# Optimization experiments

Hardware: AMD Instinct MI355X
Metric: run time of the kernel (lower is better)

Reference implementation:

```python
import jax, jax.numpy as jnp
import numpy as np

BM = 192  # query block size (kernel hard-coded to BM=192)


def setup_inputs() -> dict:
    key = jax.random.key(0)
    k1, k2, k3 = jax.random.split(key, 3)
    B, H, S, D = 1, 12, 3840, 128
    q = jax.random.normal(k1, (B, H, S, D), dtype=jnp.float32)
    k = jax.random.normal(k2, (B, H, S, D), dtype=jnp.float32)
    v = jax.random.normal(k3, (B, H, S, D), dtype=jnp.float32)
    topk = 1024
    return {"q": q, "k": k, "v": v, "topk": topk}


def reference(q, k, v, topk):
    # Chipmunk SparseDiffAttn core pipeline:
    # 1) dense_colsum_attn: dense attention whose probs are column-summed per
    #    192-query block to produce block scores bs [B,H,QG,S]
    # 2) topk index selection per query group (mask -> indices)
    # 3) csp_attn: block-sparse attention where each 192-query group attends
    #    only to its selected top-k keys
    B, H, S, D = q.shape
    QG = S // BM
    scale = 1.0 / np.sqrt(D)

    # --- dense colsum attention (scoring pass) ---
    scores = jnp.einsum('bhqd,bhkd->bhqk', q, k) * scale      # [B,H,S,S]
    probs = jax.nn.softmax(scores, axis=-1)                   # [B,H,S,S]
    # column-sum of attention probs within each 192-query block
    bs = probs.reshape(B, H, QG, BM, S).sum(axis=-2)          # [B,H,QG,S]

    # --- topk mask -> per-group key indices ---
    _, inds = jax.lax.top_k(bs, topk)                         # [B,H,QG,TK] int32

    # --- block-sparse gather attention (csp_attn) ---
    # gather selected keys/values per query group
    gather = jax.vmap(jax.vmap(lambda kv, idx: kv[idx]))      # over B, H
    kg = gather(k, inds)                                      # [B,H,QG,TK,D]
    vg = gather(v, inds)                                      # [B,H,QG,TK,D]
    qg = q.reshape(B, H, QG, BM, D)                           # [B,H,QG,BM,D]

    s2 = jnp.einsum('bhgqd,bhgkd->bhgqk', qg, kg) * scale     # [B,H,QG,BM,TK]
    p2 = jax.nn.softmax(s2, axis=-1)
    o = jnp.einsum('bhgqk,bhgkd->bhgqd', p2, vg)              # [B,H,QG,BM,D]
    return o.reshape(B, H, S, D)
```

## Files before the change

kernel.cpp:

```cpp
#include <hip/hip_runtime.h>
#include <math.h>


#define HH 12
#define SS 3840
#define DD 128
#define QGn 20
#define TKn 1024
#define NROWS (HH * QGn)
#define HS (HH * SS)
#define NT 60
#define TCH 3072
#define SCALE_D 0.08838834764831845
#define SCALE_F 0.08838834764831845f

typedef short short8 __attribute__((ext_vector_type(8)));
typedef float f32x4 __attribute__((ext_vector_type(4)));

#define MFMA(a, b, c) __builtin_amdgcn_mfma_f32_16x16x32_bf16(a, b, c, 0, 0, 0)
#define MFMA_B16(c, a, b) \
  c = __builtin_amdgcn_mfma_f32_16x16x32_bf16(a, b, c, 0, 0, 0)

typedef __attribute__((address_space(3))) unsigned int lds_u32;
typedef const __attribute__((address_space(1))) unsigned int glb_u32;

__device__ __forceinline__ unsigned short bf_rne(float x) {
  unsigned u = __float_as_uint(x);
  u = (u + 0x7fffu + ((u >> 16) & 1u)) >> 16;
  return (unsigned short)u;
}
__device__ __forceinline__ float bf_f(unsigned short b) {
  return __uint_as_float(((unsigned)b) << 16);
}
__device__ __forceinline__ void split3(float f, unsigned short& a,
                                       unsigned short& b, unsigned short& c) {
  a = bf_rne(f);
  float r = f - bf_f(a);
  b = bf_rne(r);
  r = r - bf_f(b);
  c = bf_rne(r);
}
__device__ __forceinline__ void split2(float f, unsigned short& a,
                                       unsigned short& b) {
  a = bf_rne(f);
  float r = f - bf_f(a);
  b = bf_rne(r);
}
__device__ __forceinline__ short8 ldfrag(const unsigned short* base, int chunk) {
  return *(const short8*)&base[(size_t)chunk * 8];
}

__global__ __launch_bounds__(1024) void presplit_kernel(
    const float* __restrict__ q, const float* __restrict__ k,
    unsigned short* __restrict__ qsplit, unsigned short* __restrict__ ksplit) {
  const int t = threadIdx.x;
  const int lane = t & 63;
  const int u = t >> 6;
  const int kc = u & 3, kt = u >> 2;
  const int ln = lane & 15, quad = lane >> 4;
  const int c = blockIdx.x;
  const int h = blockIdx.y;
  const float* src = blockIdx.z ? k : q;
  unsigned short* dst = blockIdx.z ? ksplit : qsplit;

  const float* p =
      &src[(size_t)(h * SS + c * 64 + kt * 16 + ln) * DD + kc * 32 + quad * 8];
  float b8[8];
  *(float4*)&b8[0] = *(const float4*)&p[0];
  *(float4*)&b8[4] = *(const float4*)&p[4];
  unsigned short f0[8], f1[8], f2[8];
#pragma unroll
  for (int e = 0; e < 8; ++e) split3(b8[e], f0[e], f1[e], f2[e]);
  size_t base =
      ((size_t)(h * NT + c) * TCH + ((kt * 4 + kc) * 3) * 64 + lane) * 8;
  *(ushort4*)&dst[base + 0] = *(ushort4*)&f0[0];
  *(ushort4*)&dst[base + 4] = *(ushort4*)&f0[4];
  *(ushort4*)&dst[base + 512] = *(ushort4*)&f1[0];
  *(ushort4*)&dst[base + 516] = *(ushort4*)&f1[4];
  *(ushort4*)&dst[base + 1024] = *(ushort4*)&f2[0];
  *(ushort4*)&dst[base + 1028] = *(ushort4*)&f2[4];
}

__global__ __launch_bounds__(256) void stats_mfma(
    const unsigned short* __restrict__ qsplit,
    const unsigned short* __restrict__ ksplit,
    double* __restrict__ lpart) {
  __shared__ __align__(16) unsigned short Bs[3][6144];
  const int t = threadIdx.x;
  const int w = t >> 6;
  const int lane = t & 63;
  const int ln = lane & 15;
  const int quad = lane >> 4;
  const int h = blockIdx.y;
  const int nq = blockIdx.z;
  const int q0 = blockIdx.x * 128 + w * 32;
  const int tq = blockIdx.x * 2 + (w >> 1);
  const int ktA = (w & 1) * 2;

  short8 A[2][4][3];
  {
    const unsigned short* qb = &qsplit[(size_t)(h * NT + tq) * TCH * 8];
#pragma unroll
    for (int s = 0; s < 2; ++s)
#pragma unroll
      for (int kc = 0; kc < 4; ++kc)
#pragma unroll
        for (int cm = 0; cm < 3; ++cm)
          A[s][kc][cm] =
              ldfrag(qb, (((ktA + s) * 4 + kc) * 3 + cm) * 64 + lane);
  }

  double racc[2][4];
#pragma unroll
  for (int s = 0; s < 2; ++s)
#pragma unroll
    for (int r = 0; r < 4; ++r) racc[s][r] = 0.0;

  const unsigned short* kq = &ksplit[(size_t)(h * NT + nq * 15) * TCH * 8];

#define STG_S(slot, j)                                                     \
  do {                                                                     \
    const unsigned short* src_ = kq + (size_t)(j) * 6144 + t * 8;          \
    __builtin_amdgcn_global_load_lds((glb_u32*)(src_),                     \
        (lds_u32*)&Bs[slot][w * 512], 16, 0, 0);                           \
    __builtin_amdgcn_global_load_lds((glb_u32*)(src_ + 2048),              \
        (lds_u32*)&Bs[slot][2048 + w * 512], 16, 0, 0);                    \
    __builtin_amdgcn_global_load_lds((glb_u32*)(src_ + 4096),              \
        (lds_u32*)&Bs[slot][4096 + w * 512], 16, 0, 0);                    \
  } while (0)

  const f32x4 z = {0.f, 0.f, 0.f, 0.f};
  f32x4 C[2][3];

  STG_S(0, 0);

  int cur = 0;
#pragma unroll 1
  for (int j = 0; j < 60; ++j) {
    __builtin_amdgcn_sched_barrier(0);
    if (j < 59) {
      const int nxt = (cur == 2) ? 0 : cur + 1;
      STG_S(nxt, j + 1);
      asm volatile("s_waitcnt vmcnt(3)" ::: "memory");
    } else {
      asm volatile("s_waitcnt vmcnt(0)" ::: "memory");
    }
    __builtin_amdgcn_s_barrier();
    __builtin_amdgcn_sched_barrier(0);
    __builtin_amdgcn_s_setprio(1);
    if (j > 0) {
#pragma unroll
      for (int s = 0; s < 2; ++s)
#pragma unroll
        for (int r = 0; r < 4; ++r) {
          float sv = (C[s][0][r] + C[s][1][r]) + C[s][2][r];
          racc[s][r] += (double)__expf(sv * SCALE_F);
        }
    }
    const unsigned short* Bp = &Bs[cur][0];
#pragma unroll
    for (int kc = 0; kc < 4; ++kc) {
      short8 B0 = *(const short8*)&Bp[(kc * 3 + 0) * 512 + lane * 8];
      short8 B1 = *(const short8*)&Bp[(kc * 3 + 1) * 512 + lane * 8];
      short8 B2 = *(const short8*)&Bp[(kc * 3 + 2) * 512 + lane * 8];
#pragma unroll
      for (int s = 0; s < 2; ++s) {
        if (kc == 0) {
          C[s][0] = MFMA(A[s][0][0], B0, z);
          C[s][1] = MFMA(A[s][0][0], B1, z);
          C[s][1] = MFMA(A[s][0][1], B0, C[s][1]);
          C[s][0] = MFMA(A[s][0][1], B1, C[s][0]);
          C[s][2] = MFMA(A[s][0][2], B0, z);
          C[s][2] = MFMA(A[s][0][0], B2, C[s][2]);
        } else {
          MFMA_B16(C[s][0], A[s][kc][0], B0);
          MFMA_B16(C[s][1], A[s][kc][0], B1);
          MFMA_B16(C[s][1], A[s][kc][1], B0);
          MFMA_B16(C[s][0], A[s][kc][1], B1);
          MFMA_B16(C[s][2], A[s][kc][2], B0);
          MFMA_B16(C[s][2], A[s][kc][0], B2);
        }
      }
    }
    __builtin_amdgcn_s_setprio(0);
    cur = (cur == 2) ? 0 : cur + 1;
  }
#undef STG_S

#pragma unroll
  for (int s = 0; s < 2; ++s)
#pragma unroll
    for (int r = 0; r < 4; ++r) {
      float sv = (C[s][0][r] + C[s][1][r]) + C[s][2][r];
      racc[s][r] += (double)__expf(sv * SCALE_F);
    }

#pragma unroll
  for (int s = 0; s < 2; ++s)
#pragma unroll
    for (int r = 0; r < 4; ++r) {
      double v = racc[s][r];
      v += __shfl_xor(v, 1);
      v += __shfl_xor(v, 2);
      v += __shfl_xor(v, 4);
      v += __shfl_xor(v, 8);
      if (ln == 0)
        lpart[(size_t)nq * HS + h * SS + q0 + s * 16 + quad * 4 + r] = v;
    }
}

__global__ __launch_bounds__(256) void colsum_mfma(
    const unsigned short* __restrict__ qsplit,
    const unsigned short* __restrict__ ksplit,
    const double* __restrict__ lpart, double* __restrict__ bs) {
  __shared__ double rls[192];
  __shared__ __align__(16) unsigned short As[3][6144];
  const int t = threadIdx.x;
  const int w = t >> 6;
  const int lane = t & 63;
  const int ln = lane & 15;
  const int quad = lane >> 4;
  const int h = blockIdx.z, g = blockIdx.y;
  const int k0 = blockIdx.x * 128 + w * 32;
  const int tk = blockIdx.x * 2 + (w >> 1);
  const int ktB = (w & 1) * 2;

  short8 Bk[2][4][3];
  {
    const unsigned short* kb = &ksplit[(size_t)(h * NT + tk) * TCH * 8];
#pragma unroll
    for (int s = 0; s < 2; ++s)
#pragma unroll
      for (int kc = 0; kc < 4; ++kc)
#pragma unroll
        for (int cm = 0; cm < 3; ++cm)
          Bk[s][kc][cm] =
              ldfrag(kb, (((ktB + s) * 4 + kc) * 3 + cm) * 64 + lane);
  }

  if (t < 192) {
    size_t qi = h * SS + g * 192 + t;
    rls[t] = 1.0 / (lpart[qi] + lpart[HS + qi] + lpart[2 * (size_t)HS + qi] +
                    lpart[3 * (size_t)HS + qi]);
  }
  __syncthreads();

  double cacc[2] = {0.0, 0.0};

  const unsigned short* qg = &qsplit[(size_t)(h * NT + g * 3) * TCH * 8];

#define STG_C(slot, j)                                                     \
  do {                                                                     \
    const unsigned short* src_ = qg + (size_t)(j) * 6144 + t * 8;          \
    __builtin_amdgcn_global_load_lds((glb_u32*)(src_),                     \
        (lds_u32*)&As[slot][w * 512], 16, 0, 0);                           \
    __builtin_amdgcn_global_load_lds((glb_u32*)(src_ + 2048),              \
        (lds_u32*)&As[slot][2048 + w * 512], 16, 0, 0);                    \
    __builtin_amdgcn_global_load_lds((glb_u32*)(src_ + 4096),              \
        (lds_u32*)&As[slot][4096 + w * 512], 16, 0, 0);                    \
  } while (0)

  const f32x4 z = {0.f, 0.f, 0.f, 0.f};
  f32x4 C[2][3];

  STG_C(0, 0);

  int cur = 0;
#pragma unroll 1
  for (int j = 0; j < 12; ++j) {
    __builtin_amdgcn_sched_barrier(0);
    if (j < 11) {
      const int nxt = (cur == 2) ? 0 : cur + 1;
      STG_C(nxt, j + 1);
      asm volatile("s_waitcnt vmcnt(3)" ::: "memory");
    } else {
      asm volatile("s_waitcnt vmcnt(0)" ::: "memory");
    }
    __builtin_amdgcn_s_barrier();
    __builtin_amdgcn_sched_barrier(0);
    __builtin_amdgcn_s_setprio(1);
    if (j > 0) {
      const int qprev = (j - 1) * 16;
#pragma unroll
      for (int s = 0; s < 2; ++s)
#pragma unroll
        for (int r = 0; r < 4; ++r) {
          float p = __expf(((C[s][0][r] + C[s][1][r]) + C[s][2][r]) * SCALE_F);
          cacc[s] += (double)p * rls[qprev + quad * 4 + r];
        }
    }
    const unsigned short* Ap = &As[cur][0];
#pragma unroll
    for (int kc = 0; kc < 4; ++kc) {
      short8 A0 = *(const short8*)&Ap[(kc * 3 + 0) * 512 + lane * 8];
      short8 A1 = *(const short8*)&Ap[(kc * 3 + 1) * 512 + lane * 8];
      short8 A2 = *(const short8*)&Ap[(kc * 3 + 2) * 512 + lane * 8];
#pragma unroll
      for (int s = 0; s < 2; ++s) {
        if (kc == 0) {
          C[s][0] = MFMA(A0, Bk[s][0][0], z);
          C[s][1] = MFMA(A1, Bk[s][0][0], z);
          C[s][1] = MFMA(A0, Bk[s][0][1], C[s][1]);
          C[s][0] = MFMA(A1, Bk[s][0][1], C[s][0]);
          C[s][2] = MFMA(A2, Bk[s][0][0], z);
          C[s][2] = MFMA(A0, Bk[s][0][2], C[s][2]);
        } else {
          MFMA_B16(C[s][0], A0, Bk[s][kc][0]);
          MFMA_B16(C[s][1], A1, Bk[s][kc][0]);
          MFMA_B16(C[s][1], A0, Bk[s][kc][1]);
          MFMA_B16(C[s][0], A1, Bk[s][kc][1]);
          MFMA_B16(C[s][2], A2, Bk[s][kc][0]);
          MFMA_B16(C[s][2], A0, Bk[s][kc][2]);
        }
      }
    }
    __builtin_amdgcn_s_setprio(0);
    cur = (cur == 2) ? 0 : cur + 1;
  }
#undef STG_C

#pragma unroll
  for (int s = 0; s < 2; ++s)
#pragma unroll
    for (int r = 0; r < 4; ++r) {
      float p = __expf(((C[s][0][r] + C[s][1][r]) + C[s][2][r]) * SCALE_F);
      cacc[s] += (double)p * rls[176 + quad * 4 + r];
    }

#pragma unroll
  for (int s = 0; s < 2; ++s) {
    double v = cacc[s];
    v += __shfl_xor(v, 16);
    v += __shfl_xor(v, 32);
    if (quad == 0)
      bs[(size_t)(h * QGn + g) * SS + k0 + s * 16 + ln] = v;
  }
}

__global__ __launch_bounds__(256) void topk3_kernel(
    const double* __restrict__ bs, int* __restrict__ inds,
    double* __restrict__ bnd_val, int* __restrict__ bnd_idx) {
  __shared__ unsigned long long u[SS];
  __shared__ int hist[256];
  __shared__ int sfx[256];
  __shared__ int s_bin, s_r;
  __shared__ int c_gt, c_eq;
  __shared__ unsigned long long rv[256];
  __shared__ int ri[256];
  const int t = threadIdx.x;
  const int row = blockIdx.x;
  const double* vals = bs + (size_t)row * SS;

  for (int i = t; i < SS; i += 256)
    u[i] = (unsigned long long)__double_as_longlong(vals[i]);

  unsigned long long pref = 0ull;
  int r = TKn;
  for (int shift = 56; shift >= 0; shift -= 8) {
    hist[t] = 0;
    __syncthreads();
    unsigned long long himask =
        (shift == 56) ? 0ull : (0xFFFFFFFFFFFFFFFFull << (shift + 8));
    for (int i = t; i < SS; i += 256) {
      unsigned long long uv = u[i];
      if ((uv & himask) == (pref & himask))
        atomicAdd(&hist[(int)((uv >> shift) & 255)], 1);
    }
    __syncthreads();
    sfx[t] = hist[t];
    __syncthreads();
#pragma unroll
    for (int off = 1; off < 256; off <<= 1) {
      int v = (t + off < 256) ? sfx[t + off] : 0;
      __syncthreads();
      sfx[t] += v;
      __syncthreads();
    }
    {
      int St = sfx[t];
      int Sn = (t == 255) ? 0 : sfx[t + 1];
      if (St >= r && Sn < r) {
        s_bin = t;
        s_r = r - Sn;
      }
    }
    if (t == 0) {
      c_gt = 0;
      c_eq = 0;
    }
    __syncthreads();
    pref |= ((unsigned long long)s_bin) << shift;
    r = s_r;
    __syncthreads();
  }
  const int G = TKn - r;
  int* out = inds + (size_t)row * TKn;
  unsigned long long mb = 0ull;
  int mbi = -1;
  for (int i = t; i < SS; i += 256) {
    unsigned long long uv = u[i];
    if (uv > pref) {
      int p = atomicAdd(&c_gt, 1);
      out[p] = i;
    } else if (uv == pref) {
      int e = atomicAdd(&c_eq, 1);
      if (e < r) out[G + e] = i;
      if (e == r - 1) bnd_idx[row * 2 + 0] = i;
    } else if (uv > mb) {
      mb = uv;
      mbi = i;
    }
  }
  rv[t] = mb;
  ri[t] = mbi;
  __syncthreads();
  for (int s2 = 128; s2 > 0; s2 >>= 1) {
    if (t < s2 && rv[t + s2] > rv[t]) {
      rv[t] = rv[t + s2];
      ri[t] = ri[t + s2];
    }
    __syncthreads();
  }
  if (t == 0) {
    bnd_val[row * 2 + 0] = __longlong_as_double((long long)pref);
    bnd_val[row * 2 + 1] = __longlong_as_double((long long)rv[0]);
    bnd_idx[row * 2 + 1] = ri[0];
  }
}

__global__ __launch_bounds__(256) void argmin_kernel(
    const double* __restrict__ bnd_val, const int* __restrict__ bnd_idx,
    int* __restrict__ rsel) {
  __shared__ double gmin[256];
  __shared__ int grow[256];
  const int t = threadIdx.x;
  double g = 1e300;
  int r = -1;
  if (t < NROWS) {
    g = bnd_val[t * 2 + 0] - bnd_val[t * 2 + 1];
    r = t;
  }
  gmin[t] = g;
  grow[t] = r;
  __syncthreads();
  for (int s2 = 128; s2 > 0; s2 >>= 1) {
    if (t < s2 && gmin[t + s2] < gmin[t]) {
      gmin[t] = gmin[t + s2];
      grow[t] = grow[t + s2];
    }
    __syncthreads();
  }
  if (t == 0) {
    int rr = grow[0];
    rsel[0] = rr;
    rsel[1] = bnd_idx[rr * 2 + 0];
    rsel[2] = bnd_idx[rr * 2 + 1];
  }
}

__global__ __launch_bounds__(256) void exact_rl_kernel(
    const float* __restrict__ q, const float* __restrict__ k,
    const int* __restrict__ rsel, double* __restrict__ rl_exact) {
  __shared__ double qd[DD];
  __shared__ double red[256];
  const int t = threadIdx.x;
  const int row = rsel[0];
  const int h = row / QGn, g = row % QGn;
  const float* qp = &q[(size_t)(h * SS + g * 192 + blockIdx.x) * DD];
  if (t < DD) qd[t] = (double)qp[t];
  __syncthreads();
  double l = 0.0;
  for (int kk = t; kk < SS; kk += 256) {
    const float* kp = &k[(size_t)(h * SS + kk) * DD];
    double s = 0.0;
#pragma unroll 4
    for (int d = 0; d < DD; d += 4) {
      float4 kv = *(const float4*)&kp[d];
      s += qd[d] * (double)kv.x + qd[d + 1] * (double)kv.y +
           qd[d + 2] * (double)kv.z + qd[d + 3] * (double)kv.w;
    }
    l += exp(s * SCALE_D);
  }
  red[t] = l;
  __syncthreads();
  for (int s2 = 128; s2 > 0; s2 >>= 1) {
    if (t < s2) red[t] += red[t + s2];
    __syncthreads();
  }
  if (t == 0) rl_exact[blockIdx.x] = 1.0 / red[0];
}

__global__ __launch_bounds__(256) void exact_pair_kernel(
    const float* __restrict__ q, const float* __restrict__ k,
    const int* __restrict__ rsel, const double* __restrict__ rl_exact,
    int* __restrict__ inds) {
  __shared__ double redX[256], redY[256];
  const int t = threadIdx.x;
  const int row = rsel[0], kept = rsel[1], drop = rsel[2];
  const int h = row / QGn, g = row % QGn;
  double px = 0.0, py = 0.0;
  if (t < 192) {
    const float* qp = &q[(size_t)(h * SS + g * 192 + t) * DD];
    const float* kx = &k[(size_t)(h * SS + kept) * DD];
    const float* ky = &k[(size_t)(h * SS + drop) * DD];
    double sx = 0.0, sy = 0.0;
#pragma unroll 4
    for (int d = 0; d < DD; ++d) {
      double qv = (double)qp[d];
      sx += qv * (double)kx[d];
      sy += qv * (double)ky[d];
    }
    double rv = rl_exact[t];
    px = exp(sx * SCALE_D) * rv;
    py = exp(sy * SCALE_D) * rv;
  }
  redX[t] = px;
  redY[t] = py;
  __syncthreads();
  for (int s2 = 128; s2 > 0; s2 >>= 1) {
    if (t < s2) { redX[t] += redX[t + s2]; redY[t] += redY[t + s2]; }
    __syncthreads();
  }
  if (t == 0)
    inds[(size_t)row * TKn + (TKn - 1)] = (redX[0] <= redY[0]) ? kept : drop;
}

__global__ __launch_bounds__(256, 3) void sparse_attn_mfma(
    const float* __restrict__ q, const float* __restrict__ v,
    const int* __restrict__ inds, const unsigned short* __restrict__ ksplit,
    float* __restrict__ out) {
  __shared__ __align__(16) unsigned short ksmN[16 * 512];
  __shared__ unsigned short vsm[2][128][40];
  __shared__ unsigned short pbuf[4][2][16][40];
  const int t = threadIdx.x;
  const int w = t >> 6;
  const int lane = t & 63;
  const int ln = lane & 15;
  const int quad = lane >> 4;
  const int h = blockIdx.z, g = blockIdx.y;
  const int qbase = g * 192 + blockIdx.x * 64;
  const int* ip = &inds[(size_t)(h * QGn + g) * TKn];
  const unsigned short* kbh = &ksplit[(size_t)(h * NT) * (TCH * 8)];

  short8 A[4][2];
  {
    const float* qp = &q[(size_t)(h * SS + qbase + w * 16 + ln) * DD + quad * 8];
#pragma unroll
    for (int kc = 0; kc < 4; ++kc) {
      float b8[8];
      *(float4*)&b8[0] = *(const float4*)&qp[kc * 32];
      *(float4*)&b8[4] = *(const float4*)&qp[kc * 32 + 4];
      short8 f0, f1;
#pragma unroll
      for (int e = 0; e < 8; ++e) {
        unsigned short x0, x1;
        split2(b8[e], x0, x1);
        f0[e] = (short)x0; f1[e] = (short)x1;
      }
      A[kc][0] = f0; A[kc][1] = f1;
    }
  }

  f32x4 O[8];
#pragma unroll
  for (int dt = 0; dt < 8; ++dt) O[dt] = (f32x4){0.f, 0.f, 0.f, 0.f};
  float lacc[4] = {0.f, 0.f, 0.f, 0.f};

  const int kk = t >> 3;
  const int sub = t & 7;
  const int sW = w >> 1;
  const int c0 = w * 4;

  int gkA = ip[sW * 16 + ln];
  float4 rv4[4];
  {
    int gkV = ip[kk];
    const float* vp = &v[(size_t)(h * SS + gkV) * DD + sub * 16];
#pragma unroll
    for (int e4 = 0; e4 < 4; ++e4) rv4[e4] = *(const float4*)&vp[e4 * 4];
  }

  for (int kt = 0; kt < TKn; kt += 32) {
    __builtin_amdgcn_s_barrier();
    __builtin_amdgcn_sched_barrier(0);
    const bool more = (kt + 32 < TKn);
    int gkVn = 0, gkAn = 0;
    if (more) {
      gkVn = ip[kt + 32 + kk];
      gkAn = ip[kt + 32 + sW * 16 + ln];
    }
    {
      const unsigned short* rowp = kbh + (size_t)(gkA >> 6) * (TCH * 8) +
                                   ((gkA & 15) + 16 * quad) * 8;
      const int ktile = (gkA >> 4) & 3;
#pragma unroll
      for (int i = 0; i < 4; ++i) {
        const int c16 = c0 + i;
        const int kc = (c16 >> 1) & 3;
        const int cm = c16 & 1;
        __builtin_amdgcn_global_load_lds(
            (glb_u32*)(rowp + ((ktile * 4 + kc) * 3 + cm) * 512),
            (lds_u32*)&ksmN[c16 * 512], 16, 0, 0);
      }
    }
#pragma unroll
    for (int e4 = 0; e4 < 4; ++e4) {
      float4 vv = rv4[e4];
      ushort4 v0, v1;
      split2(vv.x, v0.x, v1.x);
      split2(vv.y, v0.y, v1.y);
      split2(vv.z, v0.z, v1.z);
      split2(vv.w, v0.w, v1.w);
      int d0 = sub * 16 + e4 * 4;
      vsm[0][d0 + 0][kk] = v0.x; vsm[1][d0 + 0][kk] = v1.x;
      vsm[0][d0 + 1][kk] = v0.y; vsm[1][d0 + 1][kk] = v1.y;
      vsm[0][d0 + 2][kk] = v0.z; vsm[1][d0 + 2][kk] = v1.z;
      vsm[0][d0 + 3][kk] = v0.w; vsm[1][d0 + 3][kk] = v1.w;
    }
    if (more) {
      const float* vp = &v[(size_t)(h * SS + gkVn) * DD + sub * 16];
#pragma unroll
      for (int e4 = 0; e4 < 4; ++e4) rv4[e4] = *(const float4*)&vp[e4 * 4];
      asm volatile("s_waitcnt vmcnt(4) lgkmcnt(0)" ::: "memory");
      gkA = gkAn;
    } else {
      asm volatile("s_waitcnt vmcnt(0) lgkmcnt(0)" ::: "memory");
    }
    __builtin_amdgcn_s_barrier();
    __builtin_amdgcn_sched_barrier(0);

#pragma unroll
    for (int s = 0; s < 2; ++s) {
      f32x4 C0 = {0.f, 0.f, 0.f, 0.f};
      f32x4 C1 = C0;
      __builtin_amdgcn_s_setprio(1);
#pragma unroll
      for (int kc = 0; kc < 4; ++kc) {
        short8 B0 = *(const short8*)&ksmN[(s * 8 + kc * 2 + 0) * 512 + lane * 8];
        short8 B1 = *(const short8*)&ksmN[(s * 8 + kc * 2 + 1) * 512 + lane * 8];
        MFMA_B16(C0, A[kc][0], B0);
        MFMA_B16(C1, A[kc][1], B0);
        MFMA_B16(C1, A[kc][0], B1);
      }
      __builtin_amdgcn_s_setprio(0);
#pragma unroll
      for (int r = 0; r < 4; ++r) {
        float pv = __expf((C0[r] + C1[r]) * SCALE_F);
        lacc[r] += pv;
        unsigned short p0, p1;
        split2(pv, p0, p1);
        pbuf[w][0][quad * 4 + r][s * 16 + ln] = p0;
        pbuf[w][1][quad * 4 + r][s * 16 + ln] = p1;
      }
    }
    short8 P0 = *(const short8*)&pbuf[w][0][ln][quad * 8];
    short8 P1 = *(const short8*)&pbuf[w][1][ln][quad * 8];
    __builtin_amdgcn_s_setprio(1);
#pragma unroll
    for (int dt = 0; dt < 8; ++dt) {
      short8 V0 = *(const short8*)&vsm[0][dt * 16 + ln][quad * 8];
      short8 V1 = *(const short8*)&vsm[1][dt * 16 + ln][quad * 8];
      MFMA_B16(O[dt], P0, V0);
      MFMA_B16(O[dt], P1, V0);
      MFMA_B16(O[dt], P0, V1);
    }
    __builtin_amdgcn_s_setprio(0);
  }

#pragma unroll
  for (int r = 0; r < 4; ++r) {
    float l = lacc[r];
    l += __shfl_xor(l, 1);
    l += __shfl_xor(l, 2);
    l += __shfl_xor(l, 4);
    l += __shfl_xor(l, 8);
    float rl = 1.f / l;
    float* op = &out[(size_t)(h * SS + qbase + w * 16 + quad * 4 + r) * DD];
#pragma unroll
    for (int dt = 0; dt < 8; ++dt) op[dt * 16 + ln] = O[dt][r] * rl;
  }
}

extern "C" void kernel_launch(void* const* d_in, const int* in_sizes, int n_in,
                              void* d_out, int out_size, void* d_ws, size_t ws_size,
                              hipStream_t stream) {
  const float* q = (const float*)d_in[0];
  const float* k = (const float*)d_in[1];
  const float* v = (const float*)d_in[2];
  float* out = (float*)d_out;

  const size_t SPLIT_ELEMS = (size_t)HH * NT * TCH * 8;
  unsigned short* qsplit = (unsigned short*)d_ws;
  unsigned short* ksplit = qsplit + SPLIT_ELEMS;
  double* lpart = (double*)(ksplit + SPLIT_ELEMS);
  double* bs = lpart + 4 * (size_t)HS;
  int* inds = (int*)(bs + (size_t)HH * QGn * SS);
  double* bnd_val = (double*)(inds + (size_t)NROWS * TKn);
  int* bnd_idx = (int*)(bnd_val + (size_t)NROWS * 2);
  int* rsel = bnd_idx + NROWS * 2;
  double* rl_exact = (double*)(rsel + 4);

  presplit_kernel<<<dim3(NT, HH, 2), 1024, 0, stream>>>(q, k, qsplit, ksplit);
  stats_mfma<<<dim3(SS / 128, HH, 4), 256, 0, stream>>>(qsplit, ksplit, lpart);
  colsum_mfma<<<dim3(SS / 128, QGn, HH), 256, 0, stream>>>(qsplit, ksplit, lpart, bs);
  topk3_kernel<<<dim3(NROWS), 256, 0, stream>>>(bs, inds, bnd_val, bnd_idx);
  argmin_kernel<<<dim3(1), 256, 0, stream>>>(bnd_val, bnd_idx, rsel);
  exact_rl_kernel<<<dim3(192), 256, 0, stream>>>(q, k, rsel, rl_exact);
  exact_pair_kernel<<<dim3(1), 256, 0, stream>>>(q, k, rsel, rl_exact, inds);
  sparse_attn_mfma<<<dim3(3, QGn, HH), 256, 0, stream>>>(q, v, inds, ksplit, out);
}
```

Before: 781.5 us.

## Merge three query sub-blocks into one 768-thread block sharing K/V tiles

The sparse attention kernel now launches one 12-wave block per 192-query group instead of three 4-wave blocks. Only the first four waves load the gathered K and V tiles into LDS, and all twelve waves consume them, so the repeated gather traffic for the three sub-blocks is removed. The P buffer is resized per wave and read with two half-width loads. In exchange, the grid has a third as many blocks, and the barriers now synchronize twelve waves, some of which only wait while loading runs.

Result: faster. 720.9 us (-7.8%).

```diff
diff --git a/kernel.cpp b/kernel.cpp
--- a/kernel.cpp
+++ b/kernel.cpp
@@ -15,6 +15,7 @@
 #define SCALE_F 0.08838834764831845f
 
 typedef short short8 __attribute__((ext_vector_type(8)));
+typedef short short4v __attribute__((ext_vector_type(4)));
 typedef float f32x4 __attribute__((ext_vector_type(4)));
 
 #define MFMA(a, b, c) __builtin_amdgcn_mfma_f32_16x16x32_bf16(a, b, c, 0, 0, 0)
@@ -525,26 +526,26 @@
     inds[(size_t)row * TKn + (TKn - 1)] = (redX[0] <= redY[0]) ? kept : drop;
 }
 
-__global__ __launch_bounds__(256, 3) void sparse_attn_mfma(
+__global__ __launch_bounds__(768, 3) void sparse_attn_mfma(
     const float* __restrict__ q, const float* __restrict__ v,
     const int* __restrict__ inds, const unsigned short* __restrict__ ksplit,
     float* __restrict__ out) {
   __shared__ __align__(16) unsigned short ksmN[16 * 512];
-  __shared__ unsigned short vsm[2][128][40];
-  __shared__ unsigned short pbuf[4][2][16][40];
+  __shared__ __align__(16) unsigned short vsm[2][128][40];
+  __shared__ __align__(16) unsigned short pbuf[12][2][16][36];
   const int t = threadIdx.x;
   const int w = t >> 6;
   const int lane = t & 63;
   const int ln = lane & 15;
   const int quad = lane >> 4;
-  const int h = blockIdx.z, g = blockIdx.y;
-  const int qbase = g * 192 + blockIdx.x * 64;
+  const int g = blockIdx.x, h = blockIdx.y;
   const int* ip = &inds[(size_t)(h * QGn + g) * TKn];
   const unsigned short* kbh = &ksplit[(size_t)(h * NT) * (TCH * 8)];
 
   short8 A[4][2];
   {
-    const float* qp = &q[(size_t)(h * SS + qbase + w * 16 + ln) * DD + quad * 8];
+    const float* qp =
+        &q[(size_t)(h * SS + g * 192 + w * 16 + ln) * DD + quad * 8];
 #pragma unroll
     for (int kc = 0; kc < 4; ++kc) {
       float b8[8];
@@ -571,9 +572,10 @@
   const int sW = w >> 1;
   const int c0 = w * 4;
 
-  int gkA = ip[sW * 16 + ln];
+  int gkA = 0;
   float4 rv4[4];
-  {
+  if (w < 4) {
+    gkA = ip[sW * 16 + ln];
     int gkV = ip[kk];
     const float* vp = &v[(size_t)(h * SS + gkV) * DD + sub * 16];
 #pragma unroll
@@ -583,48 +585,50 @@
   for (int kt = 0; kt < TKn; kt += 32) {
     __builtin_amdgcn_s_barrier();
     __builtin_amdgcn_sched_barrier(0);
-    const bool more = (kt + 32 < TKn);
-    int gkVn = 0, gkAn = 0;
-    if (more) {
-      gkVn = ip[kt + 32 + kk];
-      gkAn = ip[kt + 32 + sW * 16 + ln];
-    }
-    {
-      const unsigned short* rowp = kbh + (size_t)(gkA >> 6) * (TCH * 8) +
-                                   ((gkA & 15) + 16 * quad) * 8;
-      const int ktile = (gkA >> 4) & 3;
-#pragma unroll
-      for (int i = 0; i < 4; ++i) {
-        const int c16 = c0 + i;
-        const int kc = (c16 >> 1) & 3;
-        const int cm = c16 & 1;
-        __builtin_amdgcn_global_load_lds(
-            (glb_u32*)(rowp + ((ktile * 4 + kc) * 3 + cm) * 512),
-            (lds_u32*)&ksmN[c16 * 512], 16, 0, 0);
-      }
-    }
-#pragma unroll
-    for (int e4 = 0; e4 < 4; ++e4) {
-      float4 vv = rv4[e4];
-      ushort4 v0, v1;
-      split2(vv.x, v0.x, v1.x);
-      split2(vv.y, v0.y, v1.y);
-      split2(vv.z, v0.z, v1.z);
-      split2(vv.w, v0.w, v1.w);
-      int d0 = sub * 16 + e4 * 4;
-      vsm[0][d0 + 0][kk] = v0.x; vsm[1][d0 + 0][kk] = v1.x;
-      vsm[0][d0 + 1][kk] = v0.y; vsm[1][d0 + 1][kk] = v1.y;
-      vsm[0][d0 + 2][kk] = v0.z; vsm[1][d0 + 2][kk] = v1.z;
-      vsm[0][d0 + 3][kk] = v0.w; vsm[1][d0 + 3][kk] = v1.w;
-    }
-    if (more) {
-      const float* vp = &v[(size_t)(h * SS + gkVn) * DD + sub * 16];
-#pragma unroll
-      for (int e4 = 0; e4 < 4; ++e4) rv4[e4] = *(const float4*)&vp[e4 * 4];
-      asm volatile("s_waitcnt vmcnt(4) lgkmcnt(0)" ::: "memory");
-      gkA = gkAn;
-    } else {
-      asm volatile("s_waitcnt vmcnt(0) lgkmcnt(0)" ::: "memory");
+    if (w < 4) {
+      const bool more = (kt + 32 < TKn);
+      int gkVn = 0, gkAn = 0;
+      if (more) {
+        gkVn = ip[kt + 32 + kk];
+        gkAn = ip[kt + 32 + sW * 16 + ln];
+      }
+      {
+        const unsigned short* rowp = kbh + (size_t)(gkA >> 6) * (TCH * 8) +
+                                     ((gkA & 15) + 16 * quad) * 8;
+        const int ktile = (gkA >> 4) & 3;
+#pragma unroll
+        for (int i = 0; i < 4; ++i) {
+          const int c16 = c0 + i;
+          const int kc = (c16 >> 1) & 3;
+          const int cm = c16 & 1;
+          __builtin_amdgcn_global_load_lds(
+              (glb_u32*)(rowp + ((ktile * 4 + kc) * 3 + cm) * 512),
+              (lds_u32*)&ksmN[c16 * 512], 16, 0, 0);
+        }
+      }
+#pragma unroll
+      for (int e4 = 0; e4 < 4; ++e4) {
+        float4 vv = rv4[e4];
+        ushort4 v0, v1;
+        split2(vv.x, v0.x, v1.x);
+        split2(vv.y, v0.y, v1.y);
+        split2(vv.z, v0.z, v1.z);
+        split2(vv.w, v0.w, v1.w);
+        int d0 = sub * 16 + e4 * 4;
+        vsm[0][d0 + 0][kk] = v0.x; vsm[1][d0 + 0][kk] = v1.x;
+        vsm[0][d0 + 1][kk] = v0.y; vsm[1][d0 + 1][kk] = v1.y;
+        vsm[0][d0 + 2][kk] = v0.z; vsm[1][d0 + 2][kk] = v1.z;
+        vsm[0][d0 + 3][kk] = v0.w; vsm[1][d0 + 3][kk] = v1.w;
+      }
+      if (more) {
+        const float* vp = &v[(size_t)(h * SS + gkVn) * DD + sub * 16];
+#pragma unroll
+        for (int e4 = 0; e4 < 4; ++e4) rv4[e4] = *(const float4*)&vp[e4 * 4];
+        asm volatile("s_waitcnt vmcnt(4) lgkmcnt(0)" ::: "memory");
+        gkA = gkAn;
+      } else {
+        asm volatile("s_waitcnt vmcnt(0) lgkmcnt(0)" ::: "memory");
+      }
     }
     __builtin_amdgcn_s_barrier();
     __builtin_amdgcn_sched_barrier(0);
@@ -653,8 +657,17 @@
         pbuf[w][1][quad * 4 + r][s * 16 + ln] = p1;
       }
     }
-    short8 P0 = *(const short8*)&pbuf[w][0][ln][quad * 8];
-    short8 P1 = *(const short8*)&pbuf[w][1][ln][quad * 8];
+    short8 P0, P1;
+    {
+      const unsigned short* pb0 = &pbuf[w][0][ln][quad * 8];
+      const unsigned short* pb1 = &pbuf[w][1][ln][quad * 8];
+      short4v lo0 = *(const short4v*)pb0;
+      short4v hi0 = *(const short4v*)(pb0 + 4);
+      short4v lo1 = *(const short4v*)pb1;
+      short4v hi1 = *(const short4v*)(pb1 + 4);
+      P0 = __builtin_shufflevector(lo0, hi0, 0, 1, 2, 3, 4, 5, 6, 7);
+      P1 = __builtin_shufflevector(lo1, hi1, 0, 1, 2, 3, 4, 5, 6, 7);
+    }
     __builtin_amdgcn_s_setprio(1);
 #pragma unroll
     for (int dt = 0; dt < 8; ++dt) {
@@ -675,7 +688,8 @@
     l += __shfl_xor(l, 4);
     l += __shfl_xor(l, 8);
     float rl = 1.f / l;
-    float* op = &out[(size_t)(h * SS + qbase + w * 16 + quad * 4 + r) * DD];
+    float* op =
+        &out[(size_t)(h * SS + g * 192 + w * 16 + quad * 4 + r) * DD];
 #pragma unroll
     for (int dt = 0; dt < 8; ++dt) op[dt * 16 + ln] = O[dt][r] * rl;
   }
@@ -707,5 +721,5 @@
   argmin_kernel<<<dim3(1), 256, 0, stream>>>(bnd_val, bnd_idx, rsel);
   exact_rl_kernel<<<dim3(192), 256, 0, stream>>>(q, k, rsel, rl_exact);
   exact_pair_kernel<<<dim3(1), 256, 0, stream>>>(q, k, rsel, rl_exact, inds);
-  sparse_attn_mfma<<<dim3(3, QGn, HH), 256, 0, stream>>>(q, v, inds, ksplit, out);
-}
+  sparse_attn_mfma<<<dim3(QGn, HH), 768, 0, stream>>>(q, v, inds, ksplit, out);
+}
```
